# Kernel optimization log

Hardware: AMD Instinct MI355X
Metric: run time of the kernel (lower is better)

The kernel has to match this reference:

```python
import jax, jax.numpy as jnp
import numpy as np

B, N, IN_DIM, OUT_DIM, HEADS = 32, 10, 65536, 64, 8
D = OUT_DIM // HEADS  # = 8; torch.matmul only typechecks because D == HEADS


def setup_inputs() -> dict:
    key = jax.random.key(0)
    k1, k2, k3 = jax.random.split(key, 3)
    x = jax.random.normal(k1, (B, N, IN_DIM), dtype=jnp.float32)
    adj = jax.random.uniform(k2, (B, N, N), dtype=jnp.float32)
    # nn.Linear(in_dim, out_dim, bias=False) weight has shape (out_dim, in_dim)
    W = jax.random.normal(k3, (OUT_DIM, IN_DIM), dtype=jnp.float32) / np.float32(np.sqrt(IN_DIM))
    return {"x": x, "adj": adj, "W": W}


def reference(x, adj, W):
    b, n, _ = x.shape
    # W(x): (B, N, out_dim) -> view (B, N, heads, D)
    xt = (x @ W.T).reshape(b, n, HEADS, D)
    # torch.matmul(x_transformed, adj_expanded) with adj_expanded[b,n,k,m] = adj[b,n,m]
    # => result[b,n,h,m] = sum_k xt[b,n,h,k] * adj[b,n,m]
    result = jnp.einsum('bnhk,bnm->bnhm', xt, adj)
    result = result.reshape(32, 10, -1)  # hardcoded in the original module
    return jax.nn.relu(result)
```

## Files before the change

kernel.cpp:

```cpp
#include <hip/hip_runtime.h>
#include <hip/hip_bf16.h>

#define BB 32
#define NN 10
#define IN_DIM 65536
#define HEADS 8
#define DD 8
#define ROWS (BB*NN)
#define MTILES (ROWS/16)
#define KBLOCKS (IN_DIM/32)
#define KSPLITS 256
#define KB_PER_SPLIT (KBLOCKS/KSPLITS)
#define KGRPS (KSPLITS/4)

typedef __attribute__((ext_vector_type(8))) short bf16x8;
typedef __attribute__((ext_vector_type(4))) float f32x4;

static __device__ __forceinline__ short f2bf(float f) {
    __hip_bfloat16 h = __float2bfloat16(f);
    return *reinterpret_cast<short*>(&h);
}

__global__ __launch_bounds__(256) void wreduce_kernel(const float* __restrict__ W,
                                                      bf16x8* __restrict__ Bfrag) {
    int tid    = blockIdx.x * 256 + threadIdx.x;
    int kblock = tid >> 6;
    int lane   = tid & 63;
    int head   = lane & 15;
    int kq     = lane >> 4;
    bf16x8 o = {0,0,0,0,0,0,0,0};
    if (head < HEADS) {
        float s0=0,s1=0,s2=0,s3=0,s4=0,s5=0,s6=0,s7=0;
        const float* wbase = W + (size_t)(head * DD) * IN_DIM + kblock * 32 + kq * 8;
#pragma unroll
        for (int d = 0; d < DD; ++d) {
            const float4* p = (const float4*)(wbase + (size_t)d * IN_DIM);
            float4 lo = p[0], hi = p[1];
            s0 += lo.x; s1 += lo.y; s2 += lo.z; s3 += lo.w;
            s4 += hi.x; s5 += hi.y; s6 += hi.z; s7 += hi.w;
        }
        o[0]=f2bf(s0); o[1]=f2bf(s1); o[2]=f2bf(s2); o[3]=f2bf(s3);
        o[4]=f2bf(s4); o[5]=f2bf(s5); o[6]=f2bf(s6); o[7]=f2bf(s7);
    }
    Bfrag[tid] = o;
}

__global__ __launch_bounds__(256) void gemv_mfma_kernel(const float* __restrict__ x,
                                                        const bf16x8* __restrict__ Bfrag,
                                                        float* __restrict__ partials) {
    const int t     = threadIdx.x;
    const int lane  = t & 63;
    const int wave  = t >> 6;
    const int mtile = blockIdx.x >> 6;
    const int kgrp  = blockIdx.x & 63;
    const int ksplit = kgrp * 4 + wave;

    const int row = mtile * 16 + (lane & 15);
    const int kq  = lane >> 4;
    const float* xrow = x + (size_t)row * IN_DIM + kq * 8;

    f32x4 acc = {0.f, 0.f, 0.f, 0.f};
    const int kb0 = ksplit * KB_PER_SPLIT;

#pragma unroll
    for (int s = 0; s < KB_PER_SPLIT; ++s) {
        const int kb = kb0 + s;
        const float4* xa = (const float4*)(xrow + kb * 32);
        float4 lo = xa[0], hi = xa[1];
        bf16x8 a;
        a[0]=f2bf(lo.x); a[1]=f2bf(lo.y); a[2]=f2bf(lo.z); a[3]=f2bf(lo.w);
        a[4]=f2bf(hi.x); a[5]=f2bf(hi.y); a[6]=f2bf(hi.z); a[7]=f2bf(hi.w);
        bf16x8 b = Bfrag[(size_t)kb * 64 + lane];
        acc = __builtin_amdgcn_mfma_f32_16x16x32_bf16(a, b, acc, 0, 0, 0);
    }

    __shared__ float red[4][64][4];
    red[wave][lane][0] = acc[0];
    red[wave][lane][1] = acc[1];
    red[wave][lane][2] = acc[2];
    red[wave][lane][3] = acc[3];
    __syncthreads();

    const int head = lane & 15;
    if (wave == 0 && head < HEADS) {
        const int r0 = (lane >> 4) * 4;
#pragma unroll
        for (int j = 0; j < 4; ++j) {
            float v = red[0][lane][j] + red[1][lane][j]
                    + red[2][lane][j] + red[3][lane][j];
            partials[((size_t)kgrp * ROWS + (mtile * 16 + r0 + j)) * HEADS + head] = v;
        }
    }
}

__global__ __launch_bounds__(256) void finalize_kernel(const float* __restrict__ partials,
                                                       const float* __restrict__ adj,
                                                       float* __restrict__ out) {
    int t = blockIdx.x * 256 + threadIdx.x;
    if (t >= ROWS * HEADS) return;
    int bn = t >> 3;
    int h  = t & 7;
    float s = 0.f;
#pragma unroll 8
    for (int g = 0; g < KGRPS; ++g)
        s += partials[((size_t)g * ROWS + bn) * HEADS + h];
    float* o = out + bn * (HEADS * NN) + h * NN;
    const float* a = adj + bn * NN;
#pragma unroll
    for (int m = 0; m < NN; ++m) {
        float v = s * a[m];
        o[m] = v > 0.f ? v : 0.f;
    }
}

extern "C" void kernel_launch(void* const* d_in, const int* in_sizes, int n_in,
                              void* d_out, int out_size, void* d_ws, size_t ws_size,
                              hipStream_t stream) {
    const float* x   = (const float*)d_in[0];
    const float* adj = (const float*)d_in[1];
    const float* W   = (const float*)d_in[2];
    float* out = (float*)d_out;

    bf16x8* Bfrag   = (bf16x8*)d_ws;
    float* partials = (float*)(Bfrag + (size_t)KBLOCKS * 64);

    wreduce_kernel<<<(KBLOCKS * 64) / 256, 256, 0, stream>>>(W, Bfrag);

    gemv_mfma_kernel<<<MTILES * KGRPS, 256, 0, stream>>>(x, Bfrag, partials);

    finalize_kernel<<<(ROWS * HEADS + 255) / 256, 256, 0, stream>>>(partials, adj, out);
}
```

Baseline: 29.35 us.

## Fuse W head-reduction into GEMV kernel and parallelize split-K finalize

Removes the separate W-reduction kernel. Each of 512 K-group blocks now reduces its own W slice into LDS as bf16 MFMA B fragments, then its four waves loop over all 20 row tiles and reuse those fragments. Partials are written per K-group without the cross-wave LDS reduction, and finalize splits the 512-way sum across 16 thread groups with a shared-memory reduce. This drops one launch and the global round trip for B fragments. In exchange there are more partials (512 groups instead of 64) and less memory-level parallelism per block.

```diff
diff --git a/kernel.cpp b/kernel.cpp
--- a/kernel.cpp
+++ b/kernel.cpp
@@ -8,10 +8,10 @@
 #define DD 8
 #define ROWS (BB*NN)
 #define MTILES (ROWS/16)
-#define KBLOCKS (IN_DIM/32)
-#define KSPLITS 256
-#define KB_PER_SPLIT (KBLOCKS/KSPLITS)
-#define KGRPS (KSPLITS/4)
+#define KGRPS 512
+#define KB_PER_GRP 4
+#define KFLOATS (KB_PER_GRP*32)
+#define PAIRS (ROWS*HEADS)
 
 typedef __attribute__((ext_vector_type(8))) short bf16x8;
 typedef __attribute__((ext_vector_type(4))) float f32x4;
@@ -21,74 +21,94 @@
     return *reinterpret_cast<short*>(&h);
 }
 
-__global__ __launch_bounds__(256) void wreduce_kernel(const float* __restrict__ W,
-                                                      bf16x8* __restrict__ Bfrag) {
-    int tid    = blockIdx.x * 256 + threadIdx.x;
-    int kblock = tid >> 6;
-    int lane   = tid & 63;
-    int head   = lane & 15;
-    int kq     = lane >> 4;
-    bf16x8 o = {0,0,0,0,0,0,0,0};
-    if (head < HEADS) {
-        float s0=0,s1=0,s2=0,s3=0,s4=0,s5=0,s6=0,s7=0;
-        const float* wbase = W + (size_t)(head * DD) * IN_DIM + kblock * 32 + kq * 8;
+__global__ __launch_bounds__(256, 2) void gemv_fused_kernel(const float* __restrict__ x,
+                                                            const float* __restrict__ W,
+                                                            float* __restrict__ partials) {
+    const int kgrp = blockIdx.x;
+    const int t    = threadIdx.x;
+    const int lane = t & 63;
+    const int wave = t >> 6;
+
+    __shared__ bf16x8 lds_b[KB_PER_GRP][64];
+
+    {
+        const int kbl  = t >> 6;
+        const int head = lane & 15;
+        const int kq   = lane >> 4;
+        bf16x8 o = {0,0,0,0,0,0,0,0};
+        if (head < HEADS) {
+            float s0=0,s1=0,s2=0,s3=0,s4=0,s5=0,s6=0,s7=0;
+            const float* wbase = W + (size_t)(head * DD) * IN_DIM
+                               + kgrp * KFLOATS + kbl * 32 + kq * 8;
 #pragma unroll
-        for (int d = 0; d < DD; ++d) {
-            const float4* p = (const float4*)(wbase + (size_t)d * IN_DIM);
-            float4 lo = p[0], hi = p[1];
-            s0 += lo.x; s1 += lo.y; s2 += lo.z; s3 += lo.w;
-            s4 += hi.x; s5 += hi.y; s6 += hi.z; s7 += hi.w;
+            for (int d = 0; d < DD; ++d) {
+                const float4* p = (const float4*)(wbase + (size_t)d * IN_DIM);
+                float4 lo = p[0], hi = p[1];
+                s0 += lo.x; s1 += lo.y; s2 += lo.z; s3 += lo.w;
+                s4 += hi.x; s5 += hi.y; s6 += hi.z; s7 += hi.w;
+            }
+            o[0]=f2bf(s0); o[1]=f2bf(s1); o[2]=f2bf(s2); o[3]=f2bf(s3);
+            o[4]=f2bf(s4); o[5]=f2bf(s5); o[6]=f2bf(s6); o[7]=f2bf(s7);
         }
-        o[0]=f2bf(s0); o[1]=f2bf(s1); o[2]=f2bf(s2); o[3]=f2bf(s3);
-        o[4]=f2bf(s4); o[5]=f2bf(s5); o[6]=f2bf(s6); o[7]=f2bf(s7);
+        lds_b[kbl][lane] = o;
     }
-    Bfrag[tid] = o;
-}
+    __syncthreads();
 
-__global__ __launch_bounds__(256) void gemv_mfma_kernel(const float* __restrict__ x,
-                                                        const bf16x8* __restrict__ Bfrag,
-                                                        float* __restrict__ partials) {
-    const int t     = threadIdx.x;
-    const int lane  = t & 63;
-    const int wave  = t >> 6;
-    const int mtile = blockIdx.x >> 6;
-    const int kgrp  = blockIdx.x & 63;
-    const int ksplit = kgrp * 4 + wave;
+    const bf16x8 b0 = lds_b[0][lane];
+    const bf16x8 b1 = lds_b[1][lane];
+    const bf16x8 b2 = lds_b[2][lane];
+    const bf16x8 b3 = lds_b[3][lane];
 
-    const int row = mtile * 16 + (lane & 15);
-    const int kq  = lane >> 4;
-    const float* xrow = x + (size_t)row * IN_DIM + kq * 8;
-
-    f32x4 acc = {0.f, 0.f, 0.f, 0.f};
-    const int kb0 = ksplit * KB_PER_SPLIT;
+    const int kq   = lane >> 4;
+    const int head = lane & 15;
+    const int r0   = (lane >> 4) * 4;
+    const size_t xoff = (size_t)kgrp * KFLOATS + kq * 8;
+    float* pbase = partials + (size_t)kgrp * PAIRS;
 
 #pragma unroll
-    for (int s = 0; s < KB_PER_SPLIT; ++s) {
-        const int kb = kb0 + s;
-        const float4* xa = (const float4*)(xrow + kb * 32);
-        float4 lo = xa[0], hi = xa[1];
-        bf16x8 a;
-        a[0]=f2bf(lo.x); a[1]=f2bf(lo.y); a[2]=f2bf(lo.z); a[3]=f2bf(lo.w);
-        a[4]=f2bf(hi.x); a[5]=f2bf(hi.y); a[6]=f2bf(hi.z); a[7]=f2bf(hi.w);
-        bf16x8 b = Bfrag[(size_t)kb * 64 + lane];
-        acc = __builtin_amdgcn_mfma_f32_16x16x32_bf16(a, b, acc, 0, 0, 0);
-    }
+    for (int m = 0; m < MTILES / 4; ++m) {
+        const int mtile = wave * (MTILES / 4) + m;
+        const int row   = mtile * 16 + (lane & 15);
+        const float* xr = x + (size_t)row * IN_DIM + xoff;
 
-    __shared__ float red[4][64][4];
-    red[wave][lane][0] = acc[0];
-    red[wave][lane][1] = acc[1];
-    red[wave][lane][2] = acc[2];
-    red[wave][lane][3] = acc[3];
-    __syncthreads();
+        f32x4 acc = {0.f, 0.f, 0.f, 0.f};
+        {
+            const float4* p = (const float4*)(xr + 0 * 32);
+            float4 lo = p[0], hi = p[1];
+            bf16x8 a;
+            a[0]=f2bf(lo.x); a[1]=f2bf(lo.y); a[2]=f2bf(lo.z); a[3]=f2bf(lo.w);
+            a[4]=f2bf(hi.x); a[5]=f2bf(hi.y); a[6]=f2bf(hi.z); a[7]=f2bf(hi.w);
+            acc = __builtin_amdgcn_mfma_f32_16x16x32_bf16(a, b0, acc, 0, 0, 0);
+        }
+        {
+            const float4* p = (const float4*)(xr + 1 * 32);
+            float4 lo = p[0], hi = p[1];
+            bf16x8 a;
+            a[0]=f2bf(lo.x); a[1]=f2bf(lo.y); a[2]=f2bf(lo.z); a[3]=f2bf(lo.w);
+            a[4]=f2bf(hi.x); a[5]=f2bf(hi.y); a[6]=f2bf(hi.z); a[7]=f2bf(hi.w);
+            acc = __builtin_amdgcn_mfma_f32_16x16x32_bf16(a, b1, acc, 0, 0, 0);
+        }
+        {
+            const float4* p = (const float4*)(xr + 2 * 32);
+            float4 lo = p[0], hi = p[1];
+            bf16x8 a;
+            a[0]=f2bf(lo.x); a[1]=f2bf(lo.y); a[2]=f2bf(lo.z); a[3]=f2bf(lo.w);
+            a[4]=f2bf(hi.x); a[5]=f2bf(hi.y); a[6]=f2bf(hi.z); a[7]=f2bf(hi.w);
+            acc = __builtin_amdgcn_mfma_f32_16x16x32_bf16(a, b2, acc, 0, 0, 0);
+        }
+        {
+            const float4* p = (const float4*)(xr + 3 * 32);
+            float4 lo = p[0], hi = p[1];
+            bf16x8 a;
+            a[0]=f2bf(lo.x); a[1]=f2bf(lo.y); a[2]=f2bf(lo.z); a[3]=f2bf(lo.w);
+            a[4]=f2bf(hi.x); a[5]=f2bf(hi.y); a[6]=f2bf(hi.z); a[7]=f2bf(hi.w);
+            acc = __builtin_amdgcn_mfma_f32_16x16x32_bf16(a, b3, acc, 0, 0, 0);
+        }
 
-    const int head = lane & 15;
-    if (wave == 0 && head < HEADS) {
-        const int r0 = (lane >> 4) * 4;
+        if (head < HEADS) {
 #pragma unroll
-        for (int j = 0; j < 4; ++j) {
-            float v = red[0][lane][j] + red[1][lane][j]
-                    + red[2][lane][j] + red[3][lane][j];
-            partials[((size_t)kgrp * ROWS + (mtile * 16 + r0 + j)) * HEADS + head] = v;
+            for (int j = 0; j < 4; ++j)
+                pbase[(size_t)(mtile * 16 + r0 + j) * HEADS + head] = acc[j];
         }
     }
 }
@@ -96,20 +116,36 @@
 __global__ __launch_bounds__(256) void finalize_kernel(const float* __restrict__ partials,
                                                        const float* __restrict__ adj,
                                                        float* __restrict__ out) {
-    int t = blockIdx.x * 256 + threadIdx.x;
-    if (t >= ROWS * HEADS) return;
-    int bn = t >> 3;
-    int h  = t & 7;
+    const int b  = blockIdx.x;
+    const int t  = threadIdx.x;
+    const int pr = t & 15;
+    const int gs = t >> 4;
+    const int pair = b * 16 + pr;
+
     float s = 0.f;
+    const float* p = partials + (size_t)gs * 32 * PAIRS + pair;
 #pragma unroll 8
-    for (int g = 0; g < KGRPS; ++g)
-        s += partials[((size_t)g * ROWS + bn) * HEADS + h];
-    float* o = out + bn * (HEADS * NN) + h * NN;
-    const float* a = adj + bn * NN;
+    for (int g = 0; g < 32; ++g)
+        s += p[(size_t)g * PAIRS];
+
+    __shared__ float red[16][16];
+    red[gs][pr] = s;
+    __syncthreads();
+
+    if (t < 16) {
+        float tot = 0.f;
 #pragma unroll
-    for (int m = 0; m < NN; ++m) {
-        float v = s * a[m];
-        o[m] = v > 0.f ? v : 0.f;
+        for (int i = 0; i < 16; ++i) tot += red[i][t];
+        const int pair2 = b * 16 + t;
+        const int bn = pair2 >> 3;
+        const int h  = pair2 & 7;
+        const float* a = adj + bn * NN;
+        float* o = out + bn * (HEADS * NN) + h * NN;
+#pragma unroll
+        for (int m = 0; m < NN; ++m) {
+            float v = tot * a[m];
+            o[m] = v > 0.f ? v : 0.f;
+        }
     }
 }
 
@@ -121,12 +157,9 @@
     const float* W   = (const float*)d_in[2];
     float* out = (float*)d_out;
 
-    bf16x8* Bfrag   = (bf16x8*)d_ws;
-    float* partials = (float*)(Bfrag + (size_t)KBLOCKS * 64);
+    float* partials = (float*)d_ws;
 
-    wreduce_kernel<<<(KBLOCKS * 64) / 256, 256, 0, stream>>>(W, Bfrag);
+    gemv_fused_kernel<<<KGRPS, 256, 0, stream>>>(x, W, partials);
 
-    gemv_mfma_kernel<<<MTILES * KGRPS, 256, 0, stream>>>(x, Bfrag, partials);
-
-    finalize_kernel<<<(ROWS * HEADS + 255) / 256, 256, 0, stream>>>(partials, adj, out);
+    finalize_kernel<<<160, 256, 0, stream>>>(partials, adj, out);
 }
```

After: 25.35 us. -13.6%, faster.
